# Optimization experiments

Measured on AMD Instinct MI355X. Metric: run time of the kernel, lower is better.

## Reference

```python
import jax, jax.numpy as jnp
import numpy as np

D = 4096          # gating_input_shape == layer width == LSTM hidden
T, XDIM = 200, 64  # trajectory length, obs dim
EMB, H1 = 128, 1024  # em_base input and first hidden
NUM_LOOP = 4      # 3 loop layers + last layer (identical structure)
PRUNING_RATIO = 0.5
K = int(D * (1.0 - PRUNING_RATIO))


def setup_inputs() -> dict:
    key = jax.random.key(0)
    ks = iter(jax.random.split(key, 32))
    def p(shape, s=0.02):
        return jax.random.normal(next(ks), shape, dtype=jnp.float32) * s
    return {
        "x": jax.random.normal(next(ks), (T, XDIM), dtype=jnp.float32),
        "emb_in": jax.random.normal(next(ks), (EMB,), dtype=jnp.float32),
        # LSTM (PyTorch gate order i,f,g,o)
        "lstm_Wih": p((4 * D, XDIM)),
        "lstm_Whh": p((4 * D, D)),
        "lstm_b": p((4 * D,)),
        # em_base MLP: relu hidden, null last activation
        "em_W1": p((H1, EMB)), "em_b1": p((H1,)),
        "em_W2": p((D, H1)), "em_b2": p((D,)),
        # gating_weight_fc_0
        "fc0_W": p((D, D)), "fc0_b": p((D,)),
        # stacked [cond_fc_1..3, cond_last] and [fc_1..3, fc_last]
        "cond_W": p((NUM_LOOP, D, D)), "cond_b": p((NUM_LOOP, D)),
        "fc_W": p((NUM_LOOP, D, D)), "fc_b": p((NUM_LOOP, D)),
    }


def _lstm_last(x, Wih, Whh, b):
    def step(carry, xt):
        h, c = carry
        z = xt @ Wih.T + h @ Whh.T + b            # [4D]
        i, f, g, o = jnp.split(z, 4)
        i, f, o = jax.nn.sigmoid(i), jax.nn.sigmoid(f), jax.nn.sigmoid(o)
        g = jnp.tanh(g)
        c = f * c + i * g
        h = o * jnp.tanh(c)
        return (h, c), None
    h0 = jnp.zeros((D,), x.dtype)
    (h, _), _ = jax.lax.scan(step, (h0, h0), x)
    return h


def _bound(a):
    mn, mx = jnp.min(a), jnp.max(a)
    return (a - mn) / (mx - mn)


def _binarize(t):
    vals, idx = jax.lax.top_k(t, K)
    pruned = jnp.zeros_like(t).at[idx].set(vals)
    return jnp.where(pruned > 0, 1.0, 0.0).astype(t.dtype)


def reference(x, emb_in, lstm_Wih, lstm_Whh, lstm_b, em_W1, em_b1, em_W2, em_b2,
              fc0_W, fc0_b, cond_W, cond_b, fc_W, fc_b):
    out = _lstm_last(x, lstm_Wih, lstm_Whh, lstm_b)                  # [D]
    h = jax.nn.relu(emb_in @ em_W1.T + em_b1)
    embedding = (h @ em_W2.T + em_b2) * out                          # [D]
    activated = jax.nn.relu(embedding)
    raw = _bound(activated @ fc0_W.T + fc0_b)                        # mask 0
    masks = [raw]
    for i in range(NUM_LOOP):                                        # 3 loop layers + last
        cond = jax.nn.relu((raw @ cond_W[i].T + cond_b[i]) * embedding)
        raw = _bound(cond @ fc_W[i].T + fc_b[i])
        masks.append(raw)
    probs = jnp.stack(masks)                                         # [5, D]
    binary = jax.vmap(_binarize)(probs)                              # [5, D]
    return probs, binary
```

## Files before the change

### kernel.cpp

```cpp
#include <hip/hip_runtime.h>
#include <hip/hip_cooperative_groups.h>

namespace cg = cooperative_groups;

constexpr int kD   = 4096;
constexpr int kT   = 200;
constexpr int kX   = 64;
constexpr int kEMB = 128;
constexpr int kH1  = 1024;
constexpr int kK   = 2048;
constexpr int kBLK = 256;
constexpr int kTHR = 1024;
constexpr int kUPB = kD / kBLK;

__device__ __forceinline__ float hsum4(float4 a) { return (a.x + a.y) + (a.z + a.w); }

__device__ __forceinline__ float wave_sum(float s) {
#pragma unroll
  for (int off = 32; off > 0; off >>= 1) s += __shfl_xor(s, off, 64);
  return s;
}

__device__ __forceinline__ int wave_sum_i(int s) {
#pragma unroll
  for (int off = 32; off > 0; off >>= 1) s += __shfl_xor(s, off, 64);
  return s;
}

__device__ __forceinline__ unsigned fenc(float f) {
  unsigned u = __float_as_uint(f);
  return (u & 0x80000000u) ? ~u : (u | 0x80000000u);
}
__device__ __forceinline__ float fdec(unsigned k) {
  return __uint_as_float((k & 0x80000000u) ? (k & 0x7FFFFFFFu) : ~k);
}

__device__ __forceinline__ float mv_row(const float* __restrict__ W, int r,
                                        const float4* sh4, int lane) {
  const float4* __restrict__ W4 = (const float4*)(W + (size_t)r * kD);
  float4 a = make_float4(0.f, 0.f, 0.f, 0.f);
#pragma unroll
  for (int c = 0; c < 16; ++c) {
    float4 wv = W4[c * 64 + lane];
    float4 hv = sh4[c * 64 + lane];
    a.x = fmaf(wv.x, hv.x, a.x);
    a.y = fmaf(wv.y, hv.y, a.y);
    a.z = fmaf(wv.z, hv.z, a.z);
    a.w = fmaf(wv.w, hv.w, a.w);
  }
  return wave_sum(hsum4(a));
}

__global__ __launch_bounds__(kTHR) void mgnet(
    const float* __restrict__ x, const float* __restrict__ emb_in,
    const float* __restrict__ Wih, const float* __restrict__ Whh,
    const float* __restrict__ lb,
    const float* __restrict__ emW1, const float* __restrict__ emb1,
    const float* __restrict__ emW2, const float* __restrict__ emb2,
    const float* __restrict__ fc0W, const float* __restrict__ fc0b,
    const float* __restrict__ condW, const float* __restrict__ condb,
    const float* __restrict__ fcW, const float* __restrict__ fcb,
    float* __restrict__ ws, float* __restrict__ out) {
  cg::grid_group grid = cg::this_grid();

  __shared__ float4 sh4[kD / 4];
  __shared__ float zs[16];
  __shared__ int redi[16];

  const int bid = blockIdx.x;
  const int tid = threadIdx.x;
  const int w = tid >> 6;
  const int lane = tid & 63;

  float* h_g   = ws;
  float* h1v   = ws + kD;
  float* ebd   = h1v + kH1;
  float* actv  = ebd + kD;
  float* vecA  = actv + kD;
  float* rawv  = vecA + kD;
  float* condv = rawv + kD;
  unsigned* slots = (unsigned*)(condv + kD);

  if (bid == 0 && tid < 5) {
    slots[2 * tid] = 0xFFFFFFFFu;
    slots[2 * tid + 1] = 0u;
  }

  const int u = bid * kUPB + w;
  const float4* W4g0 = (const float4*)(Whh + (size_t)(0 * kD + u) * kD);
  const float4* W4g1 = (const float4*)(Whh + (size_t)(1 * kD + u) * kD);
  const float4* W4g2 = (const float4*)(Whh + (size_t)(2 * kD + u) * kD);
  const float4* W4g3 = (const float4*)(Whh + (size_t)(3 * kD + u) * kD);
  const float wih0 = Wih[(size_t)(0 * kD + u) * kX + lane];
  const float wih1 = Wih[(size_t)(1 * kD + u) * kX + lane];
  const float wih2 = Wih[(size_t)(2 * kD + u) * kX + lane];
  const float wih3 = Wih[(size_t)(3 * kD + u) * kX + lane];
  const float b0 = lb[0 * kD + u], b1 = lb[1 * kD + u];
  const float b2 = lb[2 * kD + u], b3 = lb[3 * kD + u];

  float cst = 0.f;
  const float4* hg4 = (const float4*)h_g;

  for (int t = 0; t < kT; ++t) {
    sh4[tid] = (t == 0) ? make_float4(0.f, 0.f, 0.f, 0.f) : hg4[tid];
    __syncthreads();

    float4 a0 = make_float4(0.f, 0.f, 0.f, 0.f), a1 = a0, a2 = a0, a3 = a0;
#pragma unroll
    for (int c = 0; c < 16; ++c) {
      const int idx = c * 64 + lane;
      const float4 hv = sh4[idx];
      const float4 w0 = W4g0[idx];
      const float4 w1 = W4g1[idx];
      const float4 w2 = W4g2[idx];
      const float4 w3 = W4g3[idx];
      a0.x = fmaf(w0.x, hv.x, a0.x); a0.y = fmaf(w0.y, hv.y, a0.y);
      a0.z = fmaf(w0.z, hv.z, a0.z); a0.w = fmaf(w0.w, hv.w, a0.w);
      a1.x = fmaf(w1.x, hv.x, a1.x); a1.y = fmaf(w1.y, hv.y, a1.y);
      a1.z = fmaf(w1.z, hv.z, a1.z); a1.w = fmaf(w1.w, hv.w, a1.w);
      a2.x = fmaf(w2.x, hv.x, a2.x); a2.y = fmaf(w2.y, hv.y, a2.y);
      a2.z = fmaf(w2.z, hv.z, a2.z); a2.w = fmaf(w2.w, hv.w, a2.w);
      a3.x = fmaf(w3.x, hv.x, a3.x); a3.y = fmaf(w3.y, hv.y, a3.y);
      a3.z = fmaf(w3.z, hv.z, a3.z); a3.w = fmaf(w3.w, hv.w, a3.w);
    }
    const float xt = x[t * kX + lane];
    float s0 = wave_sum(hsum4(a0) + wih0 * xt);
    float s1 = wave_sum(hsum4(a1) + wih1 * xt);
    float s2 = wave_sum(hsum4(a2) + wih2 * xt);
    float s3 = wave_sum(hsum4(a3) + wih3 * xt);

    const float zi = s0 + b0, zf = s1 + b1, zg = s2 + b2, zo = s3 + b3;
    const float ig = 1.f / (1.f + expf(-zi));
    const float fg = 1.f / (1.f + expf(-zf));
    const float gg = tanhf(zg);
    const float og = 1.f / (1.f + expf(-zo));
    cst = fg * cst + ig * gg;
    const float hval = og * tanhf(cst);
    if (lane == 0) h_g[u] = hval;
    grid.sync();
  }

  {
    const int gw = bid * 16 + w;
    if (gw < kH1) {
      const float w0 = emW1[(size_t)gw * kEMB + lane];
      const float w1 = emW1[(size_t)gw * kEMB + 64 + lane];
      const float s = wave_sum(fmaf(w0, emb_in[lane], w1 * emb_in[64 + lane]));
      if (lane == 0) h1v[gw] = fmaxf(s + emb1[gw], 0.f);
    }
  }
  grid.sync();
  {
    if (tid < kH1 / 4) sh4[tid] = ((const float4*)h1v)[tid];
    __syncthreads();
    const int r = bid * 16 + w;
    const float4* W4e = (const float4*)(emW2 + (size_t)r * kH1);
    float4 a = make_float4(0.f, 0.f, 0.f, 0.f);
#pragma unroll
    for (int c = 0; c < 4; ++c) {
      const float4 wv = W4e[c * 64 + lane];
      const float4 hv = sh4[c * 64 + lane];
      a.x = fmaf(wv.x, hv.x, a.x); a.y = fmaf(wv.y, hv.y, a.y);
      a.z = fmaf(wv.z, hv.z, a.z); a.w = fmaf(wv.w, hv.w, a.w);
    }
    const float s = wave_sum(hsum4(a));
    if (lane == 0) {
      const float e = (s + emb2[r]) * h_g[r];
      ebd[r] = e;
      actv[r] = fmaxf(e, 0.f);
    }
  }
  grid.sync();

  const int r = bid * 16 + w;
  const float* vsrc = actv;
  const float* Wcur = fc0W;
  const float* bcur = fc0b;
  for (int m = 0; m <= 4; ++m) {
    sh4[tid] = ((const float4*)vsrc)[tid];
    __syncthreads();
    const float z = mv_row(Wcur, r, sh4, lane) + bcur[r];
    if (lane == 0) { vecA[r] = z; zs[w] = z; }
    __syncthreads();
    if (tid == 0) {
      float mn = zs[0], mx = zs[0];
#pragma unroll
      for (int i = 1; i < 16; ++i) { mn = fminf(mn, zs[i]); mx = fmaxf(mx, zs[i]); }
      atomicMin(&slots[2 * m], fenc(mn));
      atomicMax(&slots[2 * m + 1], fenc(mx));
    }
    grid.sync();
    if (bid < 4) {
      const int i = bid * kTHR + tid;
      const float mn = fdec(slots[2 * m]);
      const float mx = fdec(slots[2 * m + 1]);
      const float val = (vecA[i] - mn) / (mx - mn);
      rawv[i] = val;
      out[m * kD + i] = val;
    }
    grid.sync();

    if (m == 4) break;
    sh4[tid] = ((const float4*)rawv)[tid];
    __syncthreads();
    const float zc = mv_row(condW + (size_t)m * kD * kD, r, sh4, lane) + condb[m * kD + r];
    if (lane == 0) condv[r] = fmaxf(zc * ebd[r], 0.f);
    grid.sync();
    vsrc = condv;
    Wcur = fcW + (size_t)m * kD * kD;
    bcur = fcb + m * kD;
  }

  if (bid < 5) {
    const float4 pv = ((const float4*)(out + bid * kD))[tid];
    const unsigned k0 = __float_as_uint(pv.x);
    const unsigned k1 = __float_as_uint(pv.y);
    const unsigned k2 = __float_as_uint(pv.z);
    const unsigned k3 = __float_as_uint(pv.w);
    unsigned cur = 0u;
    for (int bit = 31; bit >= 0; --bit) {
      const unsigned cand = cur | (1u << bit);
      int cnt = (int)(k0 >= cand) + (int)(k1 >= cand) +
                (int)(k2 >= cand) + (int)(k3 >= cand);
      cnt = wave_sum_i(cnt);
      if (lane == 0) redi[w] = cnt;
      __syncthreads();
      int total = 0;
#pragma unroll
      for (int i = 0; i < 16; ++i) total += redi[i];
      if (total >= kK) cur = cand;
      __syncthreads();
    }
    float4 bo;
    bo.x = (k0 >= cur && k0 != 0u) ? 1.f : 0.f;
    bo.y = (k1 >= cur && k1 != 0u) ? 1.f : 0.f;
    bo.z = (k2 >= cur && k2 != 0u) ? 1.f : 0.f;
    bo.w = (k3 >= cur && k3 != 0u) ? 1.f : 0.f;
    ((float4*)(out + 5 * kD + bid * kD))[tid] = bo;
  }
}

extern "C" void kernel_launch(void* const* d_in, const int* in_sizes, int n_in,
                              void* d_out, int out_size, void* d_ws, size_t ws_size,
                              hipStream_t stream) {
  const float* x     = (const float*)d_in[0];
  const float* embi  = (const float*)d_in[1];
  const float* Wih   = (const float*)d_in[2];
  const float* Whh   = (const float*)d_in[3];
  const float* lb    = (const float*)d_in[4];
  const float* emW1  = (const float*)d_in[5];
  const float* emb1  = (const float*)d_in[6];
  const float* emW2  = (const float*)d_in[7];
  const float* emb2  = (const float*)d_in[8];
  const float* fc0W  = (const float*)d_in[9];
  const float* fc0b  = (const float*)d_in[10];
  const float* condW = (const float*)d_in[11];
  const float* condb = (const float*)d_in[12];
  const float* fcW   = (const float*)d_in[13];
  const float* fcb   = (const float*)d_in[14];
  float* ws  = (float*)d_ws;
  float* out = (float*)d_out;

  void* args[] = {&x, &embi, &Wih, &Whh, &lb, &emW1, &emb1, &emW2, &emb2,
                  &fc0W, &fc0b, &condW, &condb, &fcW, &fcb, &ws, &out};
  (void)in_sizes; (void)n_in; (void)out_size; (void)ws_size;
  hipLaunchCooperativeKernel(mgnet, dim3(kBLK), dim3(kTHR), args, 0u, stream);
}
```

Before: 21.13 ms.

## Cache part of LSTM recurrent weights in registers and LDS, prefetch across grid sync

Each wave now holds 3 of its 16 column chunks of the four gate rows of Whh in registers and 2 chunks in shared memory for the whole 200-step recurrence. It also issues the global loads for 2 more chunks before the grid barrier so they arrive while the barrier waits. This cuts the per-step global/L2 weight traffic by about 7/16 and hides some load latency behind the grid sync. In exchange it uses many more registers and 128KB of extra LDS, which may spill or fail to fit alongside the existing shared buffers.

```diff
diff --git a/kernel.cpp b/kernel.cpp
--- a/kernel.cpp
+++ b/kernel.cpp
@@ -13,7 +13,18 @@
 constexpr int kTHR = 1024;
 constexpr int kUPB = kD / kBLK;
 
+constexpr int kNCH  = kD / 256;
+constexpr int kREGc = 3;
+constexpr int kLDSc = 2;
+constexpr int kSTR0 = kREGc + kLDSc;
+constexpr int kPF   = 2;
+
 __device__ __forceinline__ float hsum4(float4 a) { return (a.x + a.y) + (a.z + a.w); }
+
+__device__ __forceinline__ void fma4(float4& a, const float4 w, const float4 h) {
+  a.x = fmaf(w.x, h.x, a.x); a.y = fmaf(w.y, h.y, a.y);
+  a.z = fmaf(w.z, h.z, a.z); a.w = fmaf(w.w, h.w, a.w);
+}
 
 __device__ __forceinline__ float wave_sum(float s) {
 #pragma unroll
@@ -43,10 +54,7 @@
   for (int c = 0; c < 16; ++c) {
     float4 wv = W4[c * 64 + lane];
     float4 hv = sh4[c * 64 + lane];
-    a.x = fmaf(wv.x, hv.x, a.x);
-    a.y = fmaf(wv.y, hv.y, a.y);
-    a.z = fmaf(wv.z, hv.z, a.z);
-    a.w = fmaf(wv.w, hv.w, a.w);
+    fma4(a, wv, hv);
   }
   return wave_sum(hsum4(a));
 }
@@ -64,6 +72,7 @@
   cg::grid_group grid = cg::this_grid();
 
   __shared__ float4 sh4[kD / 4];
+  __shared__ float4 wl4[64 * (kLDSc * 64)];
   __shared__ float zs[16];
   __shared__ int redi[16];
 
@@ -87,10 +96,10 @@
   }
 
   const int u = bid * kUPB + w;
-  const float4* W4g0 = (const float4*)(Whh + (size_t)(0 * kD + u) * kD);
-  const float4* W4g1 = (const float4*)(Whh + (size_t)(1 * kD + u) * kD);
-  const float4* W4g2 = (const float4*)(Whh + (size_t)(2 * kD + u) * kD);
-  const float4* W4g3 = (const float4*)(Whh + (size_t)(3 * kD + u) * kD);
+  const float4* __restrict__ W4g0 = (const float4*)(Whh + (size_t)(0 * kD + u) * kD);
+  const float4* __restrict__ W4g1 = (const float4*)(Whh + (size_t)(1 * kD + u) * kD);
+  const float4* __restrict__ W4g2 = (const float4*)(Whh + (size_t)(2 * kD + u) * kD);
+  const float4* __restrict__ W4g3 = (const float4*)(Whh + (size_t)(3 * kD + u) * kD);
   const float wih0 = Wih[(size_t)(0 * kD + u) * kX + lane];
   const float wih1 = Wih[(size_t)(1 * kD + u) * kX + lane];
   const float wih2 = Wih[(size_t)(2 * kD + u) * kX + lane];
@@ -98,6 +107,29 @@
   const float b0 = lb[0 * kD + u], b1 = lb[1 * kD + u];
   const float b2 = lb[2 * kD + u], b3 = lb[3 * kD + u];
 
+  float4 wr0[kREGc], wr1[kREGc], wr2[kREGc], wr3[kREGc];
+#pragma unroll
+  for (int c = 0; c < kREGc; ++c) {
+    const int idx = c * 64 + lane;
+    wr0[c] = W4g0[idx]; wr1[c] = W4g1[idx]; wr2[c] = W4g2[idx]; wr3[c] = W4g3[idx];
+  }
+#pragma unroll
+  for (int c = 0; c < kLDSc; ++c) {
+    const int idx = (kREGc + c) * 64 + lane;
+    wl4[(w * 4 + 0) * (kLDSc * 64) + c * 64 + lane] = W4g0[idx];
+    wl4[(w * 4 + 1) * (kLDSc * 64) + c * 64 + lane] = W4g1[idx];
+    wl4[(w * 4 + 2) * (kLDSc * 64) + c * 64 + lane] = W4g2[idx];
+    wl4[(w * 4 + 3) * (kLDSc * 64) + c * 64 + lane] = W4g3[idx];
+  }
+
+  float4 p00, p01, p02, p03, p10, p11, p12, p13;
+  {
+    const int i0 = kSTR0 * 64 + lane;
+    const int i1 = i0 + 64;
+    p00 = W4g0[i0]; p01 = W4g1[i0]; p02 = W4g2[i0]; p03 = W4g3[i0];
+    p10 = W4g0[i1]; p11 = W4g1[i1]; p12 = W4g2[i1]; p13 = W4g3[i1];
+  }
+
   float cst = 0.f;
   const float4* hg4 = (const float4*)h_g;
 
@@ -106,23 +138,39 @@
     __syncthreads();
 
     float4 a0 = make_float4(0.f, 0.f, 0.f, 0.f), a1 = a0, a2 = a0, a3 = a0;
-#pragma unroll
-    for (int c = 0; c < 16; ++c) {
+
+    {
+      const float4 hv0 = sh4[kSTR0 * 64 + lane];
+      fma4(a0, p00, hv0); fma4(a1, p01, hv0); fma4(a2, p02, hv0); fma4(a3, p03, hv0);
+      const float4 hv1 = sh4[(kSTR0 + 1) * 64 + lane];
+      fma4(a0, p10, hv1); fma4(a1, p11, hv1); fma4(a2, p12, hv1); fma4(a3, p13, hv1);
+    }
+#pragma unroll
+    for (int c = kSTR0 + kPF; c < kNCH; ++c) {
       const int idx = c * 64 + lane;
       const float4 hv = sh4[idx];
       const float4 w0 = W4g0[idx];
       const float4 w1 = W4g1[idx];
       const float4 w2 = W4g2[idx];
       const float4 w3 = W4g3[idx];
-      a0.x = fmaf(w0.x, hv.x, a0.x); a0.y = fmaf(w0.y, hv.y, a0.y);
-      a0.z = fmaf(w0.z, hv.z, a0.z); a0.w = fmaf(w0.w, hv.w, a0.w);
-      a1.x = fmaf(w1.x, hv.x, a1.x); a1.y = fmaf(w1.y, hv.y, a1.y);
-      a1.z = fmaf(w1.z, hv.z, a1.z); a1.w = fmaf(w1.w, hv.w, a1.w);
-      a2.x = fmaf(w2.x, hv.x, a2.x); a2.y = fmaf(w2.y, hv.y, a2.y);
-      a2.z = fmaf(w2.z, hv.z, a2.z); a2.w = fmaf(w2.w, hv.w, a2.w);
-      a3.x = fmaf(w3.x, hv.x, a3.x); a3.y = fmaf(w3.y, hv.y, a3.y);
-      a3.z = fmaf(w3.z, hv.z, a3.z); a3.w = fmaf(w3.w, hv.w, a3.w);
-    }
+      fma4(a0, w0, hv); fma4(a1, w1, hv); fma4(a2, w2, hv); fma4(a3, w3, hv);
+    }
+#pragma unroll
+    for (int c = 0; c < kREGc; ++c) {
+      const float4 hv = sh4[c * 64 + lane];
+      fma4(a0, wr0[c], hv); fma4(a1, wr1[c], hv);
+      fma4(a2, wr2[c], hv); fma4(a3, wr3[c], hv);
+    }
+#pragma unroll
+    for (int c = 0; c < kLDSc; ++c) {
+      const float4 hv = sh4[(kREGc + c) * 64 + lane];
+      const float4 w0 = wl4[(w * 4 + 0) * (kLDSc * 64) + c * 64 + lane];
+      const float4 w1 = wl4[(w * 4 + 1) * (kLDSc * 64) + c * 64 + lane];
+      const float4 w2 = wl4[(w * 4 + 2) * (kLDSc * 64) + c * 64 + lane];
+      const float4 w3 = wl4[(w * 4 + 3) * (kLDSc * 64) + c * 64 + lane];
+      fma4(a0, w0, hv); fma4(a1, w1, hv); fma4(a2, w2, hv); fma4(a3, w3, hv);
+    }
+
     const float xt = x[t * kX + lane];
     float s0 = wave_sum(hsum4(a0) + wih0 * xt);
     float s1 = wave_sum(hsum4(a1) + wih1 * xt);
@@ -137,6 +185,13 @@
     cst = fg * cst + ig * gg;
     const float hval = og * tanhf(cst);
     if (lane == 0) h_g[u] = hval;
+
+    {
+      const int i0 = kSTR0 * 64 + lane;
+      const int i1 = i0 + 64;
+      p00 = W4g0[i0]; p01 = W4g1[i0]; p02 = W4g2[i0]; p03 = W4g3[i0];
+      p10 = W4g0[i1]; p11 = W4g1[i1]; p12 = W4g2[i1]; p13 = W4g3[i1];
+    }
     grid.sync();
   }
 
@@ -160,8 +215,7 @@
     for (int c = 0; c < 4; ++c) {
       const float4 wv = W4e[c * 64 + lane];
       const float4 hv = sh4[c * 64 + lane];
-      a.x = fmaf(wv.x, hv.x, a.x); a.y = fmaf(wv.y, hv.y, a.y);
-      a.z = fmaf(wv.z, hv.z, a.z); a.w = fmaf(wv.w, hv.w, a.w);
+      fma4(a, wv, hv);
     }
     const float s = wave_sum(hsum4(a));
     if (lane == 0) {
```

Result: faster. 17.45 ms (-17.4%).
